# Optimization experiments

Measured on AMD Instinct MI355X. Metric: run time of the kernel, lower is better.

Reference implementation:

```python
import jax, jax.numpy as jnp
import numpy as np

D_MODEL = 1024
NUM_HEADS = 16
D_K = D_MODEL // NUM_HEADS
C = 1.0  # Poincare ball curvature (MANIFOLD = PoincareBall(c=Curvature(1.0)))
EPS = 1e-15


def poincare_fully_connected(x, z, r, c):
    """hypll Poincare-ball fully connected layer (HNN++, Shimizu et al.).
    x: [..., in], z: [in, out], r: [out]. Returns a point in the ball, [..., out]."""
    c_sqrt = jnp.sqrt(c)
    lam = 2.0 / (1.0 - c * jnp.sum(x * x, axis=-1, keepdims=True))  # [..., 1]
    z_norm = jnp.maximum(jnp.linalg.norm(z, axis=0), EPS)  # [out]
    two_cr = 2.0 * c_sqrt * r  # [out]
    inner = x @ (z / z_norm)  # [..., out]
    # signed hyperplane distances v_k, then map back into the ball
    v = (2.0 * z_norm / c_sqrt) * jnp.arcsinh(
        c_sqrt * lam * inner * jnp.cosh(two_cr) - (lam - 1.0) * jnp.sinh(two_cr)
    )
    w = jnp.sinh(c_sqrt * v) / c_sqrt
    return w / (1.0 + jnp.sqrt(1.0 + c * jnp.sum(w * w, axis=-1, keepdims=True)))


def setup_inputs() -> dict:
    key = jax.random.key(0)
    ks = jax.random.split(key, 7)
    B, S, D = 4, 2048, D_MODEL
    x = jax.random.normal(ks[0], (B, S, D), jnp.float32)
    # place every token strictly inside the unit Poincare ball (max norm 0.7)
    x = 0.7 * x / jnp.max(jnp.linalg.norm(x, axis=-1, keepdims=True))
    scale = 1.0 / np.sqrt(D).astype(np.float32)
    return {
        "x": x,
        "z_q": jax.random.normal(ks[1], (D, D), jnp.float32) * scale,
        "b_q": jax.random.normal(ks[2], (D,), jnp.float32) * 0.01,
        "z_k": jax.random.normal(ks[3], (D, D), jnp.float32) * scale,
        "b_k": jax.random.normal(ks[4], (D,), jnp.float32) * 0.01,
        "w_v": jax.random.normal(ks[5], (D, D), jnp.float32) * scale,
        "b_v": jax.random.normal(ks[6], (D,), jnp.float32) * 0.01,
    }


def reference(x, z_q, b_q, z_k, b_k, w_v, b_v):
    B, S, D = x.shape
    Q = poincare_fully_connected(x, z_q, b_q, C)  # [B,S,D] hyperbolic projection
    K = poincare_fully_connected(x, z_k, b_k, C)  # [B,S,D]
    V = x @ w_v.T + b_v                            # [B,S,D] Euclidean nn.Linear

    def split_heads(t):  # [B,S,D] -> [B,H,S,Dk]
        return t.reshape(B, S, NUM_HEADS, D_K).transpose(0, 2, 1, 3)

    Qh, Kh, Vh = split_heads(Q), split_heads(K), split_heads(V)
    scores = jnp.einsum("bhqd,bhkd->bhqk", Qh, Kh) / np.sqrt(D_K).astype(np.float32)
    probs = jax.nn.softmax(scores, axis=-1)
    out = jnp.einsum("bhqk,bhkd->bhqd", probs, Vh)  # [B,H,S,Dk]
    return out.transpose(0, 2, 1, 3).reshape(B, S, D)
```

## Files before the change

### kernel.cpp

```cpp
#include <hip/hip_runtime.h>
#include <hip/hip_bf16.h>
#include <math.h>

#define D_MODEL 1024
#define NHEADS  16
#define DKH     64
#define BATCH   4
#define SEQ     2048
#define NTOK    (BATCH * SEQ)
#define NELEM   ((size_t)NTOK * D_MODEL)

typedef __bf16 v8bf __attribute__((ext_vector_type(8)));
typedef float  v4f  __attribute__((ext_vector_type(4)));

__device__ __forceinline__ v8bf ld_bf16x8(const ushort* p) {
    union { uint4 u; v8bf b; } cv;
    cv.u = *(const uint4*)p;
    return cv.b;
}
__device__ __forceinline__ ushort f2bf(float f) {
    __hip_bfloat16 h = __float2bfloat16(f);
    return *(ushort*)&h;
}
__device__ __forceinline__ uint cvt_pk_bf16(float lo, float hi) {
    uint r;
    asm("v_cvt_pk_bf16_f32 %0, %1, %2" : "=v"(r) : "v"(lo), "v"(hi));
    return r;
}

#define GLOAD_LDS16(gsrc, ldst)                                            \
    __builtin_amdgcn_global_load_lds(                                      \
        (const __attribute__((address_space(1))) void*)(gsrc),             \
        (__attribute__((address_space(3))) void*)(ldst), 16, 0, 0)

#define RAW_BARRIER() __builtin_amdgcn_s_barrier()

__device__ __forceinline__ float block_reduce_sum(float v, float* sbuf) {
    #pragma unroll
    for (int off = 32; off > 0; off >>= 1)
        v += __shfl_xor(v, off, 64);
    int lane = threadIdx.x & 63;
    int wid  = threadIdx.x >> 6;
    if (lane == 0) sbuf[wid] = v;
    __syncthreads();
    float total = sbuf[0] + sbuf[1] + sbuf[2] + sbuf[3];
    __syncthreads();
    return total;
}

__global__ __launch_bounds__(256) void mega_prep(const float* __restrict__ x,
                                                 const float* __restrict__ z_q,
                                                 const float* __restrict__ r_q,
                                                 const float* __restrict__ z_k,
                                                 const float* __restrict__ r_k,
                                                 const float* __restrict__ w_v,
                                                 ushort* __restrict__ xb,
                                                 float* __restrict__ lam,
                                                 ushort* __restrict__ Wcat,
                                                 float* __restrict__ aux) {
    __shared__ float tile[64][65];
    __shared__ float sbuf[4];
    int bid = blockIdx.x;
    int t = threadIdx.x;

    if (bid < 8192) {
        int n = bid;
        const float* xr = x + (size_t)n * D_MODEL;
        float4 v = *(const float4*)&xr[t * 4];
        float s = v.x * v.x + v.y * v.y + v.z * v.z + v.w * v.w;
        float xn2 = block_reduce_sum(s, sbuf);
        if (t == 0) lam[n] = 2.f / (1.f - xn2);
        ushort u[4] = {f2bf(v.x), f2bf(v.y), f2bf(v.z), f2bf(v.w)};
        *(uint2*)&xb[(size_t)n * D_MODEL + t * 4] = *(uint2*)u;
    } else if (bid < 8704) {
        int idx = bid - 8192;
        int zsel = idx >> 8;
        int rem = idx & 255;
        int m0 = (rem & 15) * 64, k0 = (rem >> 4) * 64;
        const float* z = zsel ? z_k : z_q;
        ushort* zT = Wcat + (size_t)zsel * D_MODEL * D_MODEL;
        #pragma unroll
        for (int i = 0; i < 4; ++i) {
            int r = (t >> 4) + 16 * i;
            int c = (t & 15) * 4;
            float4 v = *(const float4*)&z[(size_t)(k0 + r) * D_MODEL + m0 + c];
            tile[r][c + 0] = v.x; tile[r][c + 1] = v.y;
            tile[r][c + 2] = v.z; tile[r][c + 3] = v.w;
        }
        __syncthreads();
        #pragma unroll
        for (int i = 0; i < 2; ++i) {
            int idx2 = t + 256 * i;
            int r = idx2 >> 3;
            int c8 = idx2 & 7;
            ushort u[8];
            #pragma unroll
            for (int j = 0; j < 8; ++j)
                u[j] = f2bf(tile[c8 * 8 + j][r]);
            *(uint4*)&zT[(size_t)(m0 + r) * D_MODEL + k0 + c8 * 8] = *(uint4*)u;
        }
    } else if (bid < 9216) {
        size_t i = ((size_t)(bid - 8704) * 256 + t) * 8;
        float4 a = *(const float4*)(w_v + i);
        float4 b = *(const float4*)(w_v + i + 4);
        ushort u[8] = {f2bf(a.x), f2bf(a.y), f2bf(a.z), f2bf(a.w),
                       f2bf(b.x), f2bf(b.y), f2bf(b.z), f2bf(b.w)};
        *(uint4*)(Wcat + (size_t)2 * D_MODEL * D_MODEL + i) = *(uint4*)u;
    } else {
        int idx = bid - 9216;
        int which = idx >> 5;
        int m0 = (idx & 31) * 32;
        const float* z = which ? z_k : z_q;
        const float* r = which ? r_k : r_q;
        float* base = aux + which * 3072;
        int mloc = t & 31;
        int krow = t >> 5;
        float s = 0.f;
        #pragma unroll 8
        for (int j = 0; j < 128; ++j) {
            float zv = z[(size_t)(krow + 8 * j) * D_MODEL + m0 + mloc];
            s = fmaf(zv, zv, s);
        }
        float* red = &tile[0][0];
        red[krow * 32 + mloc] = s;
        __syncthreads();
        if (t < 32) {
            float tot = 0.f;
            #pragma unroll
            for (int g = 0; g < 8; ++g) tot += red[g * 32 + t];
            int m = m0 + t;
            float n = fmaxf(sqrtf(tot), 1e-15f);
            float tc = 2.f * r[m];
            base[m]        = coshf(tc) / n;
            base[1024 + m] = sinhf(tc);
            base[2048 + m] = 2.f * n;
        }
    }
}

__global__ __launch_bounds__(256) void gemm_fused(const ushort* __restrict__ A,
                                                  const ushort* __restrict__ W,
                                                  const float* __restrict__ bias,
                                                  ushort* __restrict__ Pq,
                                                  ushort* __restrict__ Pk,
                                                  ushort* __restrict__ VT) {
    const int K = 1024;
    __shared__ ushort As[2][128][64];
    __shared__ ushort Bs[2][128][64];
    int tid = threadIdx.x;
    int w = tid >> 6, l = tid & 63;
    int lr = l & 15, lg = l >> 4;
    int bid = blockIdx.x;
    int xcd = bid & 7, t = bid >> 3;
    int m0 = (xcd * 8 + ((t >> 2) & 7)) * 128;
    int n0 = ((t >> 5) * 4 + (t & 3)) * 128;

    v4f acc[8][2];
    #pragma unroll
    for (int i = 0; i < 8; ++i)
        #pragma unroll
        for (int j = 0; j < 2; ++j)
            acc[i][j] = (v4f){0.f, 0.f, 0.f, 0.f};

    int srow = w * 32 + (l >> 3);
    int scol = ((l & 7) ^ ((l >> 3) & 7)) * 8;

#define STAGE_G(buf, k0) do {                                                 \
        _Pragma("unroll")                                                     \
        for (int j = 0; j < 4; ++j) {                                         \
            GLOAD_LDS16(A + (size_t)(m0 + srow + j * 8) * K + (k0) + scol,    \
                        &As[buf][w * 32 + j * 8][0]);                         \
            GLOAD_LDS16(W + (size_t)(n0 + srow + j * 8) * K + (k0) + scol,    \
                        &Bs[buf][w * 32 + j * 8][0]);                         \
        }                                                                     \
    } while (0)

    int swz = (lr & 7) << 4;

    STAGE_G(0, 0);
    for (int k0 = 0; k0 < K; k0 += 64) {
        int cur = (k0 >> 6) & 1;
        if (k0 + 64 < K) {
            STAGE_G(cur ^ 1, k0 + 64);
            asm volatile("s_waitcnt vmcnt(8)" ::: "memory");
        } else {
            asm volatile("s_waitcnt vmcnt(0)" ::: "memory");
        }
        RAW_BARRIER();
        #pragma unroll
        for (int kk = 0; kk < 2; ++kk) {
            v8bf av[8], bv[2];
            #pragma unroll
            for (int i = 0; i < 8; ++i)
                av[i] = *(const v8bf*)((const char*)&As[cur][i * 16 + lr][0]
                                       + ((kk * 64 + lg * 16) ^ swz));
            #pragma unroll
            for (int j = 0; j < 2; ++j)
                bv[j] = *(const v8bf*)((const char*)&Bs[cur][w * 32 + j * 16 + lr][0]
                                       + ((kk * 64 + lg * 16) ^ swz));
            #pragma unroll
            for (int i = 0; i < 8; ++i)
                #pragma unroll
                for (int j = 0; j < 2; ++j)
                    acc[i][j] = __builtin_amdgcn_mfma_f32_16x16x32_bf16(av[i], bv[j], acc[i][j], 0, 0, 0);
        }
        RAW_BARRIER();
    }
#undef STAGE_G

    int chunk = n0 >> 10;
    #pragma unroll
    for (int i = 0; i < 8; ++i) {
        #pragma unroll
        for (int j = 0; j < 2; ++j) {
            int col = n0 + w * 32 + j * 16 + lr;
            int cl  = col & 1023;
            if (chunk < 2) {
                ushort* P = chunk ? Pk : Pq;
                #pragma unroll
                for (int reg = 0; reg < 4; ++reg) {
                    int row = m0 + i * 16 + 4 * lg + reg;
                    P[(size_t)row * D_MODEL + cl] = f2bf(acc[i][j][reg]);
                }
            } else {
                float badd = bias[cl];
                int hh = cl >> 6, dk = cl & 63;
                int row = m0 + i * 16 + 4 * lg;
                int bb = row >> 11, ss = row & 2047;
                int sp = (ss & ~63) | (ss & 0x23) | ((ss & 0x0C) << 1) | ((ss & 0x10) >> 2);
                ushort u[4];
                #pragma unroll
                for (int reg = 0; reg < 4; ++reg)
                    u[reg] = f2bf(acc[i][j][reg] + badd);
                *(uint2*)&VT[(((size_t)(bb * NHEADS + hh)) * DKH + dk) * SEQ + sp] = *(uint2*)u;
            }
        }
    }
}

__global__ __launch_bounds__(256) void poincare_epilogue2(const ushort* __restrict__ Pq,
                                                          const ushort* __restrict__ Pk,
                                                          const float* __restrict__ lam_,
                                                          const float* __restrict__ aux,
                                                          ushort* __restrict__ Qb,
                                                          ushort* __restrict__ Kb) {
    __shared__ float sbuf[4];
    int which = blockIdx.y;
    const ushort* P  = which ? Pk : Pq;
    ushort* outb     = which ? Kb : Qb;
    const float* c1_ = aux + which * 3072;
    const float* sh_ = c1_ + 1024;
    const float* tz_ = c1_ + 2048;
    float oscale = which ? 1.0f : 0.1803368801f;

    int n = blockIdx.x;
    float lam = lam_[n];
    float lm1 = lam - 1.f;
    int o = threadIdx.x * 4;
    uint2 pu = *(const uint2*)&P[(size_t)n * D_MODEL + o];
    float4 c1 = *(const float4*)&c1_[o];
    float4 sh = *(const float4*)&sh_[o];
    float4 tz = *(const float4*)&tz_[o];
    float pv[4];
    pv[0] = __uint_as_float(pu.x << 16);
    pv[1] = __uint_as_float(pu.x & 0xffff0000u);
    pv[2] = __uint_as_float(pu.y << 16);
    pv[3] = __uint_as_float(pu.y & 0xffff0000u);
    float c1v[4] = {c1.x, c1.y, c1.z, c1.w};
    float shv[4] = {sh.x, sh.y, sh.z, sh.w};
    float tzv[4] = {tz.x, tz.y, tz.z, tz.w};
    float w[4];
    float wn2 = 0.f;
    #pragma unroll
    for (int i = 0; i < 4; ++i) {
        float t  = fmaf(lam * c1v[i], pv[i], -lm1 * shv[i]);
        float at = fabsf(t);
        float u  = at + __builtin_amdgcn_sqrtf(fmaf(at, at, 1.f));
        float tl = tzv[i] * __builtin_amdgcn_logf(u);
        float e  = __builtin_amdgcn_exp2f(tl);
        float em = __builtin_amdgcn_exp2f(-tl);
        float wa = 0.5f * (e - em);
        w[i] = copysignf(wa, t);
        wn2 = fmaf(wa, wa, wn2);
    }
    wn2 = block_reduce_sum(wn2, sbuf);
    float invd = oscale / (1.f + __builtin_amdgcn_sqrtf(1.f + wn2));
    uint2 st;
    st.x = cvt_pk_bf16(w[0] * invd, w[1] * invd);
    st.y = cvt_pk_bf16(w[2] * invd, w[3] * invd);
    *(uint2*)&outb[(size_t)n * D_MODEL + o] = st;
}

__global__ __launch_bounds__(512, 4) void attn_mfma(const ushort* __restrict__ Qb,
                                                    const ushort* __restrict__ Kb,
                                                    const ushort* __restrict__ VT,
                                                    float* __restrict__ Out) {
    __shared__ ushort Klds[4][64 * 64];
    __shared__ ushort Vlds[4][64 * 64];

    int tid = threadIdx.x;
    int w = tid >> 6, l = tid & 63;
    int lr = l & 15, lg = l >> 4;

    int flat = blockIdx.x;
    int low3 = flat & 7;
    int rest = flat >> 3;
    int qx   = rest & 7;
    int g    = (rest & ~7) | low3;
    int h = g & 15, b = g >> 4;

    const ushort* Kh = Kb + (size_t)b * SEQ * D_MODEL + h * DKH;
    const ushort* Vh = VT + (size_t)(b * NHEADS + h) * DKH * SEQ;

    const ushort* qp0 = Qb + (size_t)b * SEQ * D_MODEL + h * DKH
                      + (size_t)(qx * 256 + w * 32 + lr) * D_MODEL;
    const ushort* qp1 = qp0 + (size_t)16 * D_MODEL;
    v8bf qa[2][2];
    qa[0][0] = ld_bf16x8(qp0 + lg * 8);
    qa[0][1] = ld_bf16x8(qp0 + 32 + lg * 8);
    qa[1][0] = ld_bf16x8(qp1 + lg * 8);
    qa[1][1] = ld_bf16x8(qp1 + 32 + lg * 8);

    int row = tid >> 3;
    int c8  = (tid & 7) ^ (row & 7);
    const ushort* kg = Kh + (size_t)row * D_MODEL + c8 * 8;
    const ushort* vg = Vh + (size_t)row * SEQ + c8 * 8;

#define STAGE_KV(buf, st)  do {                                              \
        GLOAD_LDS16(kg + (size_t)(st) * 64 * D_MODEL, &Klds[buf][tid * 8]);  \
        GLOAD_LDS16(vg + (st) * 64, &Vlds[buf][tid * 8]);                    \
    } while (0)

    v4f o[2][4];
    v4f den4[2];
    #pragma unroll
    for (int st = 0; st < 2; ++st) {
        den4[st] = (v4f){0.f, 0.f, 0.f, 0.f};
        #pragma unroll
        for (int i = 0; i < 4; ++i) o[st][i] = (v4f){0.f, 0.f, 0.f, 0.f};
    }
    union { uint u[4]; v8bf v; } ones;
    ones.u[0] = ones.u[1] = ones.u[2] = ones.u[3] = 0x3f803f80u;

    auto compute = [&](int buf) {
        const char* Kc = (const char*)&Klds[buf][0];
        const char* Vc = (const char*)&Vlds[buf][0];

        v4f sc[2][4];
        #pragma unroll
        for (int st = 0; st < 2; ++st)
            #pragma unroll
            for (int i = 0; i < 4; ++i) sc[st][i] = (v4f){0.f, 0.f, 0.f, 0.f};
        __builtin_amdgcn_s_setprio(1);
        #pragma unroll
        for (int f = 0; f < 2; ++f) {
            #pragma unroll
            for (int sub = 0; sub < 4; ++sub) {
                int key = sub * 16 + lr;
                v8bf kb = *(const v8bf*)(Kc + key * 128 +
                                         ((f * 64 + lg * 16) ^ ((key & 7) << 4)));
                sc[0][sub] = __builtin_amdgcn_mfma_f32_16x16x32_bf16(kb, qa[0][f], sc[0][sub], 0, 0, 0);
                sc[1][sub] = __builtin_amdgcn_mfma_f32_16x16x32_bf16(kb, qa[1][f], sc[1][sub], 0, 0, 0);
            }
        }
        __builtin_amdgcn_s_setprio(0);

        uint pk[2][8];
        #pragma unroll
        for (int st = 0; st < 2; ++st) {
            #pragma unroll
            for (int sub = 0; sub < 4; ++sub) {
                float p0 = __builtin_amdgcn_exp2f(sc[st][sub][0]);
                float p1 = __builtin_amdgcn_exp2f(sc[st][sub][1]);
                float p2 = __builtin_amdgcn_exp2f(sc[st][sub][2]);
                float p3 = __builtin_amdgcn_exp2f(sc[st][sub][3]);
                pk[st][sub * 2 + 0] = cvt_pk_bf16(p0, p1);
                pk[st][sub * 2 + 1] = cvt_pk_bf16(p2, p3);
            }
        }

        __builtin_amdgcn_s_setprio(1);
        #pragma unroll
        for (int f = 0; f < 2; ++f) {
            union { uint u[4]; v8bf v; } pa0, pa1;
            #pragma unroll
            for (int j = 0; j < 4; ++j) { pa0.u[j] = pk[0][4 * f + j]; pa1.u[j] = pk[1][4 * f + j]; }
            den4[0] = __builtin_amdgcn_mfma_f32_16x16x32_bf16(pa0.v, ones.v, den4[0], 0, 0, 0);
            den4[1] = __builtin_amdgcn_mfma_f32_16x16x32_bf16(pa1.v, ones.v, den4[1], 0, 0, 0);
            #pragma unroll
            for (int sub = 0; sub < 4; ++sub) {
                int dk = sub * 16 + lr;
                v8bf vb = *(const v8bf*)(Vc + dk * 128 +
                                         ((f * 64 + lg * 16) ^ ((dk & 7) << 4)));
                o[0][sub] = __builtin_amdgcn_mfma_f32_16x16x32_bf16(pa0.v, vb, o[0][sub], 0, 0, 0);
                o[1][sub] = __builtin_amdgcn_mfma_f32_16x16x32_bf16(pa1.v, vb, o[1][sub], 0, 0, 0);
            }
        }
        __builtin_amdgcn_s_setprio(0);
    };

    STAGE_KV(0, 0);
    STAGE_KV(1, 1);
    STAGE_KV(2, 2);

    for (int tb = 0; tb < 28; tb += 4) {
        #pragma unroll
        for (int i = 0; i < 4; ++i) {
            asm volatile("s_waitcnt vmcnt(4)" ::: "memory");
            RAW_BARRIER();
            STAGE_KV((i + 3) & 3, tb + i + 3);
            compute(i);
        }
    }
    asm volatile("s_waitcnt vmcnt(4)" ::: "memory");
    RAW_BARRIER();
    STAGE_KV(3, 31);
    compute(0);
    asm volatile("s_waitcnt vmcnt(4)" ::: "memory");
    RAW_BARRIER();
    compute(1);
    asm volatile("s_waitcnt vmcnt(2)" ::: "memory");
    RAW_BARRIER();
    compute(2);
    asm volatile("s_waitcnt vmcnt(0)" ::: "memory");
    RAW_BARRIER();
    compute(3);

    #pragma unroll
    for (int st = 0; st < 2; ++st) {
        size_t obase = (size_t)b * SEQ * D_MODEL +
                       (size_t)(qx * 256 + w * 32 + st * 16 + lg * 4) * D_MODEL + h * DKH;
        #pragma unroll
        for (int reg = 0; reg < 4; ++reg) {
            float inv = 1.f / den4[st][reg];
            #pragma unroll
            for (int sub = 0; sub < 4; ++sub)
                Out[obase + (size_t)reg * D_MODEL + sub * 16 + lr] = o[st][sub][reg] * inv;
        }
    }
#undef STAGE_KV
}

extern "C" void kernel_launch(void* const* d_in, const int* in_sizes, int n_in,
                              void* d_out, int out_size, void* d_ws, size_t ws_size,
                              hipStream_t stream) {
    const float* x   = (const float*)d_in[0];
    const float* z_q = (const float*)d_in[1];
    const float* b_q = (const float*)d_in[2];
    const float* z_k = (const float*)d_in[3];
    const float* b_k = (const float*)d_in[4];
    const float* w_v = (const float*)d_in[5];
    const float* b_v = (const float*)d_in[6];
    float* out = (float*)d_out;

    ushort* Pq   = (ushort*)d_ws;
    ushort* xb   = Pq + NELEM;
    ushort* Qb   = xb;
    ushort* Wcat = xb + NELEM;
    ushort* VT   = Wcat + (size_t)3 * D_MODEL * D_MODEL;
    ushort* Kb   = VT + NELEM;
    float*  aux  = (float*)(Kb + NELEM);
    float*  lam  = aux + 6144;
    ushort* Pk   = (ushort*)out;

    mega_prep<<<dim3(9280), 256, 0, stream>>>(x, z_q, b_q, z_k, b_k, w_v,
                                              xb, lam, Wcat, aux);

    gemm_fused<<<dim3(1536), 256, 0, stream>>>(xb, Wcat, b_v, Pq, Pk, VT);

    poincare_epilogue2<<<dim3(NTOK, 2), 256, 0, stream>>>(Pq, Pk, lam, aux, Qb, Kb);

    attn_mfma<<<dim3(512), 512, 0, stream>>>(Qb, Kb, VT, out);
}
```

Measured before the change: 160.1 us.

## Replace double-buffered LDS staging in fused GEMM with single-buffer synchronous loads

```diff
diff --git a/kernel.cpp b/kernel.cpp
--- a/kernel.cpp
+++ b/kernel.cpp
@@ -145,8 +145,8 @@
                                                   ushort* __restrict__ Pk,
                                                   ushort* __restrict__ VT) {
     const int K = 1024;
-    __shared__ ushort As[2][128][64];
-    __shared__ ushort Bs[2][128][64];
+    __shared__ ushort As[128][64];
+    __shared__ ushort Bs[128][64];
     int tid = threadIdx.x;
     int w = tid >> 6, l = tid & 63;
     int lr = l & 15, lg = l >> 4;
@@ -165,38 +165,28 @@
     int srow = w * 32 + (l >> 3);
     int scol = ((l & 7) ^ ((l >> 3) & 7)) * 8;
 
-#define STAGE_G(buf, k0) do {                                                 \
-        _Pragma("unroll")                                                     \
-        for (int j = 0; j < 4; ++j) {                                         \
-            GLOAD_LDS16(A + (size_t)(m0 + srow + j * 8) * K + (k0) + scol,    \
-                        &As[buf][w * 32 + j * 8][0]);                         \
-            GLOAD_LDS16(W + (size_t)(n0 + srow + j * 8) * K + (k0) + scol,    \
-                        &Bs[buf][w * 32 + j * 8][0]);                         \
-        }                                                                     \
-    } while (0)
-
     int swz = (lr & 7) << 4;
 
-    STAGE_G(0, 0);
     for (int k0 = 0; k0 < K; k0 += 64) {
-        int cur = (k0 >> 6) & 1;
-        if (k0 + 64 < K) {
-            STAGE_G(cur ^ 1, k0 + 64);
-            asm volatile("s_waitcnt vmcnt(8)" ::: "memory");
-        } else {
-            asm volatile("s_waitcnt vmcnt(0)" ::: "memory");
-        }
-        RAW_BARRIER();
+        #pragma unroll
+        for (int j = 0; j < 4; ++j) {
+            GLOAD_LDS16(A + (size_t)(m0 + srow + j * 8) * K + k0 + scol,
+                        &As[w * 32 + j * 8][0]);
+            GLOAD_LDS16(W + (size_t)(n0 + srow + j * 8) * K + k0 + scol,
+                        &Bs[w * 32 + j * 8][0]);
+        }
+        asm volatile("s_waitcnt vmcnt(0)" ::: "memory");
+        __syncthreads();
         #pragma unroll
         for (int kk = 0; kk < 2; ++kk) {
             v8bf av[8], bv[2];
             #pragma unroll
             for (int i = 0; i < 8; ++i)
-                av[i] = *(const v8bf*)((const char*)&As[cur][i * 16 + lr][0]
+                av[i] = *(const v8bf*)((const char*)&As[i * 16 + lr][0]
                                        + ((kk * 64 + lg * 16) ^ swz));
             #pragma unroll
             for (int j = 0; j < 2; ++j)
-                bv[j] = *(const v8bf*)((const char*)&Bs[cur][w * 32 + j * 16 + lr][0]
+                bv[j] = *(const v8bf*)((const char*)&Bs[w * 32 + j * 16 + lr][0]
                                        + ((kk * 64 + lg * 16) ^ swz));
             #pragma unroll
             for (int i = 0; i < 8; ++i)
@@ -204,9 +194,8 @@
                 for (int j = 0; j < 2; ++j)
                     acc[i][j] = __builtin_amdgcn_mfma_f32_16x16x32_bf16(av[i], bv[j], acc[i][j], 0, 0, 0);
         }
-        RAW_BARRIER();
-    }
-#undef STAGE_G
+        __syncthreads();
+    }
 
     int chunk = n0 >> 10;
     #pragma unroll
```

Measured after the change: 165.9 us. 3.6% more time.
